# Kernel tuning notes

Measured on AMD Instinct MI355X. Metric: run time of the kernel, lower is better.

Reference implementation:

```python
import jax, jax.numpy as jnp
import numpy as np

LRELU_ALPHA = 0.2
ACT_GAIN = float(np.sqrt(2.0))  # def_gain for lrelu in bias_act
UP = 2


def setup_inputs() -> dict:
    key = jax.random.key(0)
    ks = jax.random.split(key, 5)
    B, IC, OC, WD, RES, K = 16, 512, 512, 512, 64, 3
    Hin = RES // UP
    x = jax.random.normal(ks[0], (B, IC, Hin, Hin), jnp.float32)
    w = jax.random.normal(ks[1], (B, WD), jnp.float32)
    affine_weight = jax.random.normal(ks[2], (IC, WD), jnp.float32)  # torch.randn / lr_mult(=1)
    affine_bias = jnp.ones((IC,), jnp.float32)                        # bias_init=1
    conv_weight = jax.random.normal(ks[3], (OC, IC, K, K), jnp.float32)
    bias = jnp.zeros((OC,), jnp.float32)
    noise_const = jax.random.normal(ks[4], (RES, RES), jnp.float32)
    # setup_filter([1,3,3,1]): outer product, normalized to sum 1
    f1 = jnp.array([1.0, 3.0, 3.0, 1.0], jnp.float32)
    f = jnp.outer(f1, f1)
    f = f / jnp.sum(f)
    return dict(x=x, w=w, affine_weight=affine_weight, affine_bias=affine_bias,
                conv_weight=conv_weight, bias=bias, noise_const=noise_const, f=f)


def reference(x, w, affine_weight, affine_bias, conv_weight, bias, noise_const, f):
    B, IC, H, W = x.shape
    OC, _, kh, kw = conv_weight.shape
    # --- affine (FullyConnectedLayer, linear activation) ---
    wg = 1.0 / jnp.sqrt(jnp.asarray(affine_weight.shape[1], jnp.float32))
    styles = w @ (affine_weight * wg).T + affine_bias  # [B, IC]
    # --- modulate + demodulate ---
    wmod = conv_weight[None] * styles[:, None, :, None, None]      # [B,OC,IC,kh,kw]
    dcoefs = jax.lax.rsqrt(jnp.sum(jnp.square(wmod), axis=(2, 3, 4)) + 1e-8)  # [B,OC]
    wmod = wmod * dcoefs[:, :, None, None, None]
    # --- grouped (per-sample) transpose conv, stride=UP ---
    # torch conv_transpose2d(x, W[in,out], stride=up, pad=0) ==
    # dilated cross-correlation with spatially flipped OIHW kernel, pad k-1.
    wflip = jnp.flip(wmod, (3, 4))  # [B,OC,IC,kh,kw]

    def one_sample(xb, wb):
        return jax.lax.conv_general_dilated(
            xb[None], wb, window_strides=(1, 1),
            padding=[(kh - 1, kh - 1), (kw - 1, kw - 1)],
            lhs_dilation=(UP, UP),
            dimension_numbers=('NCHW', 'OIHW', 'NCHW'))[0]

    y = jax.vmap(one_sample)(x, wflip)  # [B, OC, UP*H+1, UP*W+1]
    # --- upfirdn2d: pad 1 each side, 4x4 FIR (symmetric -> flip is identity), gain=UP^2 ---
    fh, fw = f.shape
    pad = 1  # px0 = k//2 + (fw+UP-1)//2 - (kw-1) = 1 (same for all sides)
    yp = jnp.pad(y, ((0, 0), (0, 0), (pad, pad), (pad, pad)))
    Hy, Wy = yp.shape[2], yp.shape[3]
    fk = (f * (UP * UP))[None, None]  # [1,1,fh,fw]
    y = jax.lax.conv_general_dilated(
        yp.reshape(B * OC, 1, Hy, Wy), fk, (1, 1), 'VALID',
        dimension_numbers=('NCHW', 'OIHW', 'NCHW'))
    y = y.reshape(B, OC, Hy - fh + 1, Wy - fw + 1)  # [B, OC, UP*H, UP*W]
    # --- noise (const) + bias + lrelu * gain (conv_clamp=None) ---
    y = y + noise_const[None, None]
    y = y + bias[None, :, None, None]
    y = jax.nn.leaky_relu(y, LRELU_ALPHA) * ACT_GAIN
    return y
```

## Files before the change

kernel.cpp:

```cpp
#include <hip/hip_runtime.h>
#include <hip/hip_bf16.h>
#include <cstddef>
#include <cstdint>


typedef __attribute__((ext_vector_type(8))) short s16x8;
typedef __attribute__((ext_vector_type(4))) short s16x4;
typedef __attribute__((ext_vector_type(4))) float f32x4;

static __device__ __forceinline__ unsigned short f2bf(float v) {
  __hip_bfloat16 h = __float2bfloat16(v);
  return __builtin_bit_cast(unsigned short, h);
}
static __device__ __forceinline__ float bf2f(unsigned short u) {
  unsigned int x = ((unsigned int)u) << 16;
  return __builtin_bit_cast(float, x);
}

static __device__ __forceinline__ void gload16(const void* g, const void* l) {
  __builtin_amdgcn_global_load_lds((const __attribute__((address_space(1))) unsigned int*)g,
                                   (__attribute__((address_space(3))) unsigned int*)l, 16, 0, 0);
}

__global__ void k_styles(const float* __restrict__ w, const float* __restrict__ aw,
                         const float* __restrict__ ab, float* __restrict__ styles) {
  int b = blockIdx.x;
  int ic = blockIdx.y * 32 + (threadIdx.x >> 3);
  int l = threadIdx.x & 7;
  const float wg = 0.044194173824159216f;
  const float* wp = w + b * 512 + l * 64;
  const float* ap = aw + (size_t)ic * 512 + l * 64;
  float s = 0.f;
  for (int d = 0; d < 64; d += 4) {
    float4 wv = *(const float4*)(wp + d);
    float4 av = *(const float4*)(ap + d);
    s += wv.x * av.x + wv.y * av.y + wv.z * av.z + wv.w * av.w;
  }
  s += __shfl_down(s, 4, 64);
  s += __shfl_down(s, 2, 64);
  s += __shfl_down(s, 1, 64);
  if (l == 0) styles[b * 512 + ic] = s * wg + ab[ic];
}

__global__ void k_wt_dcoef(const float* __restrict__ cw, const float* __restrict__ styles,
                           unsigned short* __restrict__ wt, float* __restrict__ dcoefs,
                           int do_wt) {
  __shared__ float lw[4608];
  __shared__ float part[4][16];
  int oc = blockIdx.x, t = threadIdx.x;
  for (int k = t; k < 4608; k += 256) lw[k] = cw[(size_t)oc * 4608 + k];
  __syncthreads();
  if (do_wt) {
    for (int c = t; c < 576; c += 256) {
      int tap = c >> 6, icc = c & 63;
      s16x8 v;
#pragma unroll
      for (int e = 0; e < 8; ++e) v[e] = (short)f2bf(lw[(icc * 8 + e) * 9 + tap]);
      *(s16x8*)(wt + ((size_t)oc * 9 + tap) * 512 + icc * 8) = v;
    }
  }
  float acc[16];
#pragma unroll
  for (int b2 = 0; b2 < 16; ++b2) acc[b2] = 0.f;
#pragma unroll
  for (int j = 0; j < 2; ++j) {
    int ic = t * 2 + j;
    float s2 = 0.f;
#pragma unroll
    for (int k = 0; k < 9; ++k) { float v = lw[ic * 9 + k]; s2 += v * v; }
#pragma unroll
    for (int b2 = 0; b2 < 16; ++b2) { float s = styles[b2 * 512 + ic]; acc[b2] += s2 * s * s; }
  }
#pragma unroll
  for (int off = 32; off > 0; off >>= 1) {
#pragma unroll
    for (int b2 = 0; b2 < 16; ++b2) acc[b2] += __shfl_down(acc[b2], off, 64);
  }
  int wid = t >> 6, lane = t & 63;
  if (lane == 0) {
    for (int b2 = 0; b2 < 16; ++b2) part[wid][b2] = acc[b2];
  }
  __syncthreads();
  if (t < 16) {
    float s = part[0][t] + part[1][t] + part[2][t] + part[3][t];
    dcoefs[t * 512 + oc] = rsqrtf(s + 1e-8f);
  }
}

__global__ void k_xt(const float* __restrict__ x, const float* __restrict__ styles,
                     unsigned short* __restrict__ xtp) {
  __shared__ __align__(16) unsigned short trans[32][520];
  int pr = blockIdx.x, b = blockIdx.y, t = threadIdx.x;
  bool interior = (pr >= 2 && pr < 34);
  if (interior) {
    int iy = pr - 2;
#pragma unroll 4
    for (int i = 0; i < 64; ++i) {
      int idx = t + i * 256;
      int ic = idx >> 5, ix = idx & 31;
      float v = x[((size_t)(b * 512 + ic)) * 1024 + iy * 32 + ix] * styles[b * 512 + ic];
      trans[ix][ic] = f2bf(v);
    }
  }
  __syncthreads();
  for (int c = t; c < 2304; c += 256) {
    int pc = c >> 6, icc = c & 63;
    s16x8 v = {0, 0, 0, 0, 0, 0, 0, 0};
    if (interior && pc >= 2 && pc < 34) v = *(const s16x8*)&trans[pc - 2][icc * 8];
    *(s16x8*)(xtp + ((size_t)(b * 1296 + pr * 36 + pc)) * 512 + icc * 8) = v;
  }
}

template <int PRE>
__global__ __launch_bounds__(256, 2)
void k_main(const unsigned short* __restrict__ xtp, const unsigned short* __restrict__ wtp,
            const float* __restrict__ xg, const float* __restrict__ cw,
            const float* __restrict__ styles, const float* __restrict__ dcoefs,
            const float* __restrict__ bias, const float* __restrict__ noise,
            float* __restrict__ out) {
  __shared__ __align__(16) unsigned char smem[58368];

  int bid = blockIdx.x;
  int q8 = (bid >> 3) + (bid & 7) * 128;
  const int ocT = q8 & 15, yT = (q8 >> 4) & 3, b = q8 >> 6;
  const int oc0 = ocT * 32;
  const int J0 = yT * 8, Y0 = yT * 16;
  const int tid = threadIdx.x, wid = tid >> 6, lane = tid & 63;
  const int l15 = lane & 15, l4 = lane >> 4;

  const int fs1 = (wid < 2) ? wid * 6 : 12 + (wid - 2) * 5;
  const int NF1 = (wid < 2) ? 6 : 5;
  int bb0[5], bb1[6];
#pragma unroll
  for (int f = 0; f < 5; ++f) {
    int n = (wid * 5 + f) * 16 + l15;
    int jy = n / 34, jx = n - jy * 34;
    bb0[f] = ((jy + 1) * 36 + jx + 1) * 80 + l4 * 16;
  }
#pragma unroll
  for (int f = 0; f < 6; ++f) {
    int n = (fs1 + f) * 16 + l15;
    int jy = n / 34, jx = n - jy * 34;
    bb1[f] = ((jy + 1) * 36 + jx + 1) * 80 + l4 * 16;
  }
  const int aoffB = l15 * 80 + l4 * 16;

  f32x4 acc0[2][2][5];
  f32x4 acc1[2][2][6];
#pragma unroll
  for (int px = 0; px < 2; ++px)
#pragma unroll
    for (int mf = 0; mf < 2; ++mf) {
#pragma unroll
      for (int f = 0; f < 5; ++f) acc0[px][mf][f] = (f32x4){0.f, 0.f, 0.f, 0.f};
#pragma unroll
      for (int f = 0; f < 6; ++f) acc1[px][mf][f] = (f32x4){0.f, 0.f, 0.f, 0.f};
    }

  const char* LX = (const char*)smem;
  const char* LW = (const char*)smem + 34816;

  for (int kc = 0; kc < 16; ++kc) {
    const int ic0 = kc * 32;
    __syncthreads();
    if (PRE) {
      const unsigned short* xsb = xtp + ((size_t)(b * 1296 + J0 * 36)) * 512 + ic0;
      for (int i = wid; i < 34; i += 4) {
        int q = i * 64 + lane;
        int q2 = q < 2159 ? q : 2159;
        int run = q2 / 5;
        int c = q2 - run * 5; c = c > 3 ? 3 : c;
        gload16(xsb + run * 512 + c * 8, smem + i * 1024);
      }
      const unsigned short* wsb = wtp + (size_t)oc0 * 4608 + ic0;
      for (int i = wid; i < 23; i += 4) {
        int q = i * 64 + lane;
        int q2 = q < 1439 ? q : 1439;
        int run = q2 / 5;
        int c = q2 - run * 5; c = c > 3 ? 3 : c;
        int tap = run >> 5, ocr = run & 31;
        gload16(wsb + (size_t)ocr * 4608 + tap * 512 + c * 8, smem + 34816 + i * 1024);
      }
      asm volatile("s_waitcnt vmcnt(0)" ::: "memory");
    } else {
      for (int s = tid; s < 1728; s += 256) {
        int run = s >> 2, c = s & 3;
        int r = run / 36, cc = run - r * 36;
        int iy = J0 + r - 2, ix = cc - 2;
        s16x8 v = {0, 0, 0, 0, 0, 0, 0, 0};
        if ((unsigned)iy < 32u && (unsigned)ix < 32u) {
#pragma unroll
          for (int e = 0; e < 8; ++e) {
            int ic = ic0 + c * 8 + e;
            v[e] = (short)f2bf(xg[((size_t)(b * 512 + ic)) * 1024 + iy * 32 + ix] * styles[b * 512 + ic]);
          }
        }
        *(s16x8*)((char*)smem + run * 80 + c * 16) = v;
      }
      for (int s = tid; s < 1152; s += 256) {
        int run = s >> 2, c = s & 3;
        int tap = run >> 5, ocr = run & 31;
        s16x8 v;
#pragma unroll
        for (int e = 0; e < 8; ++e)
          v[e] = (short)f2bf(cw[((size_t)(oc0 + ocr) * 512 + ic0 + c * 8 + e) * 9 + tap]);
        *(s16x8*)((char*)smem + 34816 + run * 80 + c * 16) = v;
      }
    }
    __syncthreads();

    const char* aw_ = LW + aoffB;
    {
      s16x8 A[3][2];
#pragma unroll
      for (int kx = 0; kx < 3; ++kx)
#pragma unroll
        for (int mf = 0; mf < 2; ++mf) A[kx][mf] = *(const s16x8*)(aw_ + kx * 2560 + mf * 1280);
#pragma unroll
      for (int f = 0; f < 5; ++f) {
        const char* bp = LX + bb0[f];
        s16x8 B3 = *(const s16x8*)(bp + 2880);
        s16x8 B4 = *(const s16x8*)(bp + 2960);
#pragma unroll
        for (int mf = 0; mf < 2; ++mf) {
          acc0[0][mf][f] = __builtin_amdgcn_mfma_f32_16x16x32_bf16(A[0][mf], B4, acc0[0][mf][f], 0, 0, 0);
          acc0[0][mf][f] = __builtin_amdgcn_mfma_f32_16x16x32_bf16(A[2][mf], B3, acc0[0][mf][f], 0, 0, 0);
          acc0[1][mf][f] = __builtin_amdgcn_mfma_f32_16x16x32_bf16(A[1][mf], B3, acc0[1][mf][f], 0, 0, 0);
        }
      }
    }
    {
      s16x8 A[3][2];
#pragma unroll
      for (int kx = 0; kx < 3; ++kx)
#pragma unroll
        for (int mf = 0; mf < 2; ++mf) A[kx][mf] = *(const s16x8*)(aw_ + (6 + kx) * 2560 + mf * 1280);
#pragma unroll
      for (int f = 0; f < 5; ++f) {
        const char* bp = LX + bb0[f];
        s16x8 B1 = *(const s16x8*)(bp);
        s16x8 B2 = *(const s16x8*)(bp + 80);
#pragma unroll
        for (int mf = 0; mf < 2; ++mf) {
          acc0[0][mf][f] = __builtin_amdgcn_mfma_f32_16x16x32_bf16(A[0][mf], B2, acc0[0][mf][f], 0, 0, 0);
          acc0[0][mf][f] = __builtin_amdgcn_mfma_f32_16x16x32_bf16(A[2][mf], B1, acc0[0][mf][f], 0, 0, 0);
          acc0[1][mf][f] = __builtin_amdgcn_mfma_f32_16x16x32_bf16(A[1][mf], B1, acc0[1][mf][f], 0, 0, 0);
        }
      }
    }
    {
      s16x8 A[3][2];
#pragma unroll
      for (int kx = 0; kx < 3; ++kx)
#pragma unroll
        for (int mf = 0; mf < 2; ++mf) A[kx][mf] = *(const s16x8*)(aw_ + (3 + kx) * 2560 + mf * 1280);
#pragma unroll
      for (int f = 0; f < 6; ++f) {
        if (f < NF1) {
          const char* bp = LX + bb1[f];
          s16x8 B1 = *(const s16x8*)(bp);
          s16x8 B2 = *(const s16x8*)(bp + 80);
#pragma unroll
          for (int mf = 0; mf < 2; ++mf) {
            acc1[0][mf][f] = __builtin_amdgcn_mfma_f32_16x16x32_bf16(A[0][mf], B2, acc1[0][mf][f], 0, 0, 0);
            acc1[0][mf][f] = __builtin_amdgcn_mfma_f32_16x16x32_bf16(A[2][mf], B1, acc1[0][mf][f], 0, 0, 0);
            acc1[1][mf][f] = __builtin_amdgcn_mfma_f32_16x16x32_bf16(A[1][mf], B1, acc1[1][mf][f], 0, 0, 0);
          }
        }
      }
    }
  }

  unsigned short* ly = (unsigned short*)smem;
#pragma unroll
  for (int mf = 0; mf < 2; ++mf) {
    __syncthreads();
#pragma unroll
    for (int f = 0; f < 5; ++f) {
      int n = (wid * 5 + f) * 16 + l15;
      if (n < 306) {
        int jy = n / 34, jx = n - jy * 34;
        int yr = 2 * jy + 1;
#pragma unroll
        for (int px = 0; px < 2; ++px) {
          int yc = 2 * jx + 1 - px;
#pragma unroll
          for (int r = 0; r < 4; ++r)
            ly[(l4 * 4 + r) * 1292 + yr * 68 + yc] = f2bf(acc0[px][mf][f][r]);
        }
      }
    }
#pragma unroll
    for (int f = 0; f < 6; ++f) {
      if (f < NF1) {
        int n = (fs1 + f) * 16 + l15;
        if (n < 340) {
          int jy = n / 34, jx = n - jy * 34;
          int yr = 2 * jy;
#pragma unroll
          for (int px = 0; px < 2; ++px) {
            int yc = 2 * jx + 1 - px;
#pragma unroll
            for (int r = 0; r < 4; ++r)
              ly[(l4 * 4 + r) * 1292 + yr * 68 + yc] = f2bf(acc1[px][mf][f][r]);
          }
        }
      }
    }
    __syncthreads();
    for (int task = tid; task < 1088; task += 256) {
      int ocr = task / 68;
      int c2 = task - ocr * 68;
      unsigned short* colp = ly + ocr * 1292 + c2;
      float y0 = bf2f(colp[0]), y1 = bf2f(colp[68]), y2 = bf2f(colp[136]);
      float vt[16];
#pragma unroll
      for (int Y = 0; Y < 16; ++Y) {
        float y3 = bf2f(colp[(Y + 3) * 68]);
        vt[Y] = 0.25f * (y0 + y3) + 0.75f * (y1 + y2);
        y0 = y1; y1 = y2; y2 = y3;
      }
#pragma unroll
      for (int Y = 0; Y < 16; ++Y) colp[Y * 68] = f2bf(vt[Y]);
    }
    __syncthreads();
    for (int task = tid; task < 1024; task += 256) {
      int ocr = task >> 6, rem = task & 63;
      int Y = rem >> 2, qq = rem & 3;
      const unsigned short* rowp = ly + ocr * 1292 + Y * 68 + qq * 16;
      float vb[20];
#pragma unroll
      for (int k = 0; k < 5; ++k) {
        s16x4 ch = *(const s16x4*)(rowp + k * 4);
#pragma unroll
        for (int j2 = 0; j2 < 4; ++j2) vb[k * 4 + j2] = bf2f((unsigned short)ch[j2]);
      }
      int oc = oc0 + mf * 16 + ocr;
      int Yg = Y0 + Y, Xg = qq * 16;
      float dc = dcoefs[b * 512 + oc];
      float bv = bias[oc];
      const float* np = noise + Yg * 64 + Xg;
      float* op = out + (((size_t)(b * 512 + oc)) * 64 + Yg) * 64 + Xg;
#pragma unroll
      for (int xx = 0; xx < 16; ++xx) {
        float o = 0.25f * (vb[xx] + vb[xx + 3]) + 0.75f * (vb[xx + 1] + vb[xx + 2]);
        o = o * dc + np[xx] + bv;
        o = (o > 0.f ? o : 0.2f * o) * 1.4142135623730951f;
        op[xx] = o;
      }
    }
  }
}

extern "C" void kernel_launch(void* const* d_in, const int* in_sizes, int n_in,
                              void* d_out, int out_size, void* d_ws, size_t ws_size,
                              hipStream_t stream) {
  const float* x = (const float*)d_in[0];
  const float* w = (const float*)d_in[1];
  const float* aw = (const float*)d_in[2];
  const float* ab = (const float*)d_in[3];
  const float* cw = (const float*)d_in[4];
  const float* bias = (const float*)d_in[5];
  const float* noise = (const float*)d_in[6];
  float* out = (float*)d_out;

  float* styles = (float*)d_ws;
  float* dcoefs = styles + 8192;
  unsigned short* xtp = (unsigned short*)((char*)d_ws + 65536);
  unsigned short* wtp = xtp + (size_t)16 * 1296 * 512;
  size_t need = 65536 + (size_t)16 * 1296 * 512 * 2 + (size_t)512 * 9 * 512 * 2;
  int pre = (ws_size >= need) ? 1 : 0;

  k_styles<<<dim3(16, 16), 256, 0, stream>>>(w, aw, ab, styles);
  k_wt_dcoef<<<dim3(512), 256, 0, stream>>>(cw, styles, wtp, dcoefs, pre);
  if (pre) {
    k_xt<<<dim3(36, 16), 256, 0, stream>>>(x, styles, xtp);
    k_main<1><<<dim3(1024), 256, 0, stream>>>(xtp, wtp, x, cw, styles, dcoefs, bias, noise, out);
  } else {
    k_main<0><<<dim3(1024), 256, 0, stream>>>(xtp, wtp, x, cw, styles, dcoefs, bias, noise, out);
  }
}
```

Measured before the change: 305.4 us.

## Double-buffer activation tiles and load weights directly from fragment-ordered global layout

The main conv kernel now double-buffers the X tile in LDS, issuing the next channel chunk's async global-to-LDS loads while MFMAs run on the current chunk. Weights are no longer staged through LDS; the prep kernel writes them in an MFMA-fragment-ordered layout so each lane loads its A operand straight from global memory. Smaller changes vectorise the x transpose loads and the vertical FIR pass, which now processes two columns per 32-bit access. LDS use grows to about 69 KB, which may limit occupancy to two blocks per CU. The direct global weight loads add latency inside the compute loop.

```diff
diff --git a/kernel.cpp b/kernel.cpp
--- a/kernel.cpp
+++ b/kernel.cpp
@@ -42,21 +42,23 @@
   if (l == 0) styles[b * 512 + ic] = s * wg + ab[ic];
 }
 
-__global__ void k_wt_dcoef(const float* __restrict__ cw, const float* __restrict__ styles,
-                           unsigned short* __restrict__ wt, float* __restrict__ dcoefs,
-                           int do_wt) {
+__global__ void k_prep(const float* __restrict__ cw, const float* __restrict__ styles,
+                       unsigned short* __restrict__ wt2, float* __restrict__ dcoefs,
+                       int do_wt) {
   __shared__ float lw[4608];
   __shared__ float part[4][16];
   int oc = blockIdx.x, t = threadIdx.x;
-  for (int k = t; k < 4608; k += 256) lw[k] = cw[(size_t)oc * 4608 + k];
+  for (int k = t; k < 1152; k += 256)
+    *(float4*)(lw + k * 4) = *(const float4*)(cw + (size_t)oc * 4608 + k * 4);
   __syncthreads();
   if (do_wt) {
+    int ocT = oc >> 5, mf = (oc >> 4) & 1, l15 = oc & 15;
     for (int c = t; c < 576; c += 256) {
-      int tap = c >> 6, icc = c & 63;
+      int kc = c / 36, rem = c % 36, tap = rem >> 2, l4 = rem & 3;
       s16x8 v;
 #pragma unroll
-      for (int e = 0; e < 8; ++e) v[e] = (short)f2bf(lw[(icc * 8 + e) * 9 + tap]);
-      *(s16x8*)(wt + ((size_t)oc * 9 + tap) * 512 + icc * 8) = v;
+      for (int e = 0; e < 8; ++e) v[e] = (short)f2bf(lw[(kc * 32 + l4 * 8 + e) * 9 + tap]);
+      *(s16x8*)(wt2 + ((size_t)(((ocT * 16 + kc) * 9 + tap) * 2 + mf) * 64 + l4 * 16 + l15) * 8) = v;
     }
   }
   float acc[16];
@@ -94,12 +96,14 @@
   bool interior = (pr >= 2 && pr < 34);
   if (interior) {
     int iy = pr - 2;
-#pragma unroll 4
-    for (int i = 0; i < 64; ++i) {
-      int idx = t + i * 256;
-      int ic = idx >> 5, ix = idx & 31;
-      float v = x[((size_t)(b * 512 + ic)) * 1024 + iy * 32 + ix] * styles[b * 512 + ic];
-      trans[ix][ic] = f2bf(v);
+    for (int task = t; task < 4096; task += 256) {
+      int ic = task >> 3, q = task & 7;
+      float4 v = *(const float4*)(x + ((size_t)(b * 512 + ic)) * 1024 + iy * 32 + q * 4);
+      float s = styles[b * 512 + ic];
+      trans[q * 4 + 0][ic] = f2bf(v.x * s);
+      trans[q * 4 + 1][ic] = f2bf(v.y * s);
+      trans[q * 4 + 2][ic] = f2bf(v.z * s);
+      trans[q * 4 + 3][ic] = f2bf(v.w * s);
     }
   }
   __syncthreads();
@@ -113,12 +117,12 @@
 
 template <int PRE>
 __global__ __launch_bounds__(256, 2)
-void k_main(const unsigned short* __restrict__ xtp, const unsigned short* __restrict__ wtp,
+void k_main(const unsigned short* __restrict__ xtp, const unsigned short* __restrict__ wt2,
             const float* __restrict__ xg, const float* __restrict__ cw,
             const float* __restrict__ styles, const float* __restrict__ dcoefs,
             const float* __restrict__ bias, const float* __restrict__ noise,
             float* __restrict__ out) {
-  __shared__ __align__(16) unsigned char smem[58368];
+  __shared__ __align__(16) unsigned char smem[69120];
 
   int bid = blockIdx.x;
   int q8 = (bid >> 3) + (bid & 7) * 128;
@@ -143,7 +147,6 @@
     int jy = n / 34, jx = n - jy * 34;
     bb1[f] = ((jy + 1) * 36 + jx + 1) * 80 + l4 * 16;
   }
-  const int aoffB = l15 * 80 + l4 * 16;
 
   f32x4 acc0[2][2][5];
   f32x4 acc1[2][2][6];
@@ -157,32 +160,35 @@
       for (int f = 0; f < 6; ++f) acc1[px][mf][f] = (f32x4){0.f, 0.f, 0.f, 0.f};
     }
 
-  const char* LX = (const char*)smem;
-  const char* LW = (const char*)smem + 34816;
+  const unsigned short* xsb = xtp + ((size_t)(b * 1296 + J0 * 36)) * 512;
+
+  if (PRE) {
+    for (int i = wid; i < 34; i += 4) {
+      int q = i * 64 + lane;
+      int q2 = q < 2159 ? q : 2159;
+      int run = q2 / 5;
+      int c = q2 - run * 5; c = c > 3 ? 3 : c;
+      gload16(xsb + run * 512 + c * 8, smem + i * 1024);
+    }
+    __syncthreads();
+  }
 
   for (int kc = 0; kc < 16; ++kc) {
     const int ic0 = kc * 32;
-    __syncthreads();
     if (PRE) {
-      const unsigned short* xsb = xtp + ((size_t)(b * 1296 + J0 * 36)) * 512 + ic0;
-      for (int i = wid; i < 34; i += 4) {
-        int q = i * 64 + lane;
-        int q2 = q < 2159 ? q : 2159;
-        int run = q2 / 5;
-        int c = q2 - run * 5; c = c > 3 ? 3 : c;
-        gload16(xsb + run * 512 + c * 8, smem + i * 1024);
-      }
-      const unsigned short* wsb = wtp + (size_t)oc0 * 4608 + ic0;
-      for (int i = wid; i < 23; i += 4) {
-        int q = i * 64 + lane;
-        int q2 = q < 1439 ? q : 1439;
-        int run = q2 / 5;
-        int c = q2 - run * 5; c = c > 3 ? 3 : c;
-        int tap = run >> 5, ocr = run & 31;
-        gload16(wsb + (size_t)ocr * 4608 + tap * 512 + c * 8, smem + 34816 + i * 1024);
-      }
-      asm volatile("s_waitcnt vmcnt(0)" ::: "memory");
+      if (kc < 15) {
+        char* dst = (char*)smem + ((kc + 1) & 1) * 34560;
+        const unsigned short* src = xsb + (kc + 1) * 32;
+        for (int i = wid; i < 34; i += 4) {
+          int q = i * 64 + lane;
+          int q2 = q < 2159 ? q : 2159;
+          int run = q2 / 5;
+          int c = q2 - run * 5; c = c > 3 ? 3 : c;
+          gload16(src + run * 512 + c * 8, dst + i * 1024);
+        }
+      }
     } else {
+      __syncthreads();
       for (int s = tid; s < 1728; s += 256) {
         int run = s >> 2, c = s & 3;
         int r = run / 36, cc = run - r * 36;
@@ -197,28 +203,34 @@
         }
         *(s16x8*)((char*)smem + run * 80 + c * 16) = v;
       }
-      for (int s = tid; s < 1152; s += 256) {
-        int run = s >> 2, c = s & 3;
-        int tap = run >> 5, ocr = run & 31;
-        s16x8 v;
-#pragma unroll
-        for (int e = 0; e < 8; ++e)
-          v[e] = (short)f2bf(cw[((size_t)(oc0 + ocr) * 512 + ic0 + c * 8 + e) * 9 + tap]);
-        *(s16x8*)((char*)smem + 34816 + run * 80 + c * 16) = v;
-      }
-    }
-    __syncthreads();
-
-    const char* aw_ = LW + aoffB;
+      __syncthreads();
+    }
+
+    const char* BUF = (const char*)smem + (PRE ? (kc & 1) * 34560 : 0);
+    const unsigned short* aB = wt2 + ((size_t)(ocT * 16 + kc)) * 9 * 1024 + lane * 8;
+
+#define LOAD_A(A, TAP0)                                                                   \
+    {                                                                                     \
+      if (PRE) {                                                                          \
+        _Pragma("unroll") for (int kx = 0; kx < 3; ++kx)                                  \
+          _Pragma("unroll") for (int mf = 0; mf < 2; ++mf)                                \
+            A[kx][mf] = *(const s16x8*)(aB + ((TAP0 + kx) * 2 + mf) * 512);               \
+      } else {                                                                            \
+        _Pragma("unroll") for (int kx = 0; kx < 3; ++kx)                                  \
+          _Pragma("unroll") for (int mf = 0; mf < 2; ++mf) {                              \
+            _Pragma("unroll") for (int e = 0; e < 8; ++e)                                 \
+              A[kx][mf][e] = (short)f2bf(                                                 \
+                  cw[((size_t)(oc0 + mf * 16 + l15) * 512 + ic0 + l4 * 8 + e) * 9 + TAP0 + kx]); \
+          }                                                                               \
+      }                                                                                   \
+    }
+
     {
       s16x8 A[3][2];
-#pragma unroll
-      for (int kx = 0; kx < 3; ++kx)
-#pragma unroll
-        for (int mf = 0; mf < 2; ++mf) A[kx][mf] = *(const s16x8*)(aw_ + kx * 2560 + mf * 1280);
+      LOAD_A(A, 0)
 #pragma unroll
       for (int f = 0; f < 5; ++f) {
-        const char* bp = LX + bb0[f];
+        const char* bp = BUF + bb0[f];
         s16x8 B3 = *(const s16x8*)(bp + 2880);
         s16x8 B4 = *(const s16x8*)(bp + 2960);
 #pragma unroll
@@ -231,13 +243,10 @@
     }
     {
       s16x8 A[3][2];
-#pragma unroll
-      for (int kx = 0; kx < 3; ++kx)
-#pragma unroll
-        for (int mf = 0; mf < 2; ++mf) A[kx][mf] = *(const s16x8*)(aw_ + (6 + kx) * 2560 + mf * 1280);
+      LOAD_A(A, 6)
 #pragma unroll
       for (int f = 0; f < 5; ++f) {
-        const char* bp = LX + bb0[f];
+        const char* bp = BUF + bb0[f];
         s16x8 B1 = *(const s16x8*)(bp);
         s16x8 B2 = *(const s16x8*)(bp + 80);
 #pragma unroll
@@ -250,14 +259,11 @@
     }
     {
       s16x8 A[3][2];
-#pragma unroll
-      for (int kx = 0; kx < 3; ++kx)
-#pragma unroll
-        for (int mf = 0; mf < 2; ++mf) A[kx][mf] = *(const s16x8*)(aw_ + (3 + kx) * 2560 + mf * 1280);
+      LOAD_A(A, 3)
 #pragma unroll
       for (int f = 0; f < 6; ++f) {
         if (f < NF1) {
-          const char* bp = LX + bb1[f];
+          const char* bp = BUF + bb1[f];
           s16x8 B1 = *(const s16x8*)(bp);
           s16x8 B2 = *(const s16x8*)(bp + 80);
 #pragma unroll
@@ -269,6 +275,8 @@
         }
       }
     }
+#undef LOAD_A
+    if (PRE) __syncthreads();
   }
 
   unsigned short* ly = (unsigned short*)smem;
@@ -308,20 +316,22 @@
       }
     }
     __syncthreads();
-    for (int task = tid; task < 1088; task += 256) {
-      int ocr = task / 68;
-      int c2 = task - ocr * 68;
-      unsigned short* colp = ly + ocr * 1292 + c2;
-      float y0 = bf2f(colp[0]), y1 = bf2f(colp[68]), y2 = bf2f(colp[136]);
-      float vt[16];
+    for (int task = tid; task < 544; task += 256) {
+      int ocr = task / 34, cp = task - ocr * 34;
+      unsigned int* colp = (unsigned int*)(ly + ocr * 1292) + cp;
+      unsigned int u0 = colp[0], u1 = colp[34], u2 = colp[68];
 #pragma unroll
       for (int Y = 0; Y < 16; ++Y) {
-        float y3 = bf2f(colp[(Y + 3) * 68]);
-        vt[Y] = 0.25f * (y0 + y3) + 0.75f * (y1 + y2);
-        y0 = y1; y1 = y2; y2 = y3;
-      }
-#pragma unroll
-      for (int Y = 0; Y < 16; ++Y) colp[Y * 68] = f2bf(vt[Y]);
+        unsigned int u3 = colp[(Y + 3) * 34];
+        float a0 = bf2f((unsigned short)(u0 & 0xffff)), b0 = bf2f((unsigned short)(u0 >> 16));
+        float a1 = bf2f((unsigned short)(u1 & 0xffff)), b1 = bf2f((unsigned short)(u1 >> 16));
+        float a2 = bf2f((unsigned short)(u2 & 0xffff)), b2 = bf2f((unsigned short)(u2 >> 16));
+        float a3 = bf2f((unsigned short)(u3 & 0xffff)), b3 = bf2f((unsigned short)(u3 >> 16));
+        float va = 0.25f * (a0 + a3) + 0.75f * (a1 + a2);
+        float vb = 0.25f * (b0 + b3) + 0.75f * (b1 + b2);
+        colp[Y * 34] = (unsigned int)f2bf(va) | ((unsigned int)f2bf(vb) << 16);
+        u0 = u1; u1 = u2; u2 = u3;
+      }
     }
     __syncthreads();
     for (int task = tid; task < 1024; task += 256) {
@@ -367,16 +377,16 @@
   float* styles = (float*)d_ws;
   float* dcoefs = styles + 8192;
   unsigned short* xtp = (unsigned short*)((char*)d_ws + 65536);
-  unsigned short* wtp = xtp + (size_t)16 * 1296 * 512;
-  size_t need = 65536 + (size_t)16 * 1296 * 512 * 2 + (size_t)512 * 9 * 512 * 2;
+  unsigned short* wt2 = xtp + (size_t)16 * 1296 * 512;
+  size_t need = 65536 + (size_t)16 * 1296 * 512 * 2 + (size_t)16 * 16 * 9 * 1024 * 2;
   int pre = (ws_size >= need) ? 1 : 0;
 
   k_styles<<<dim3(16, 16), 256, 0, stream>>>(w, aw, ab, styles);
-  k_wt_dcoef<<<dim3(512), 256, 0, stream>>>(cw, styles, wtp, dcoefs, pre);
+  k_prep<<<dim3(512), 256, 0, stream>>>(cw, styles, wt2, dcoefs, pre);
   if (pre) {
     k_xt<<<dim3(36, 16), 256, 0, stream>>>(x, styles, xtp);
-    k_main<1><<<dim3(1024), 256, 0, stream>>>(xtp, wtp, x, cw, styles, dcoefs, bias, noise, out);
+    k_main<1><<<dim3(1024), 256, 0, stream>>>(xtp, wt2, x, cw, styles, dcoefs, bias, noise, out);
   } else {
-    k_main<0><<<dim3(1024), 256, 0, stream>>>(xtp, wtp, x, cw, styles, dcoefs, bias, noise, out);
-  }
-}
+    k_main<0><<<dim3(1024), 256, 0, stream>>>(xtp, wt2, x, cw, styles, dcoefs, bias, noise, out);
+  }
+}
```

New measurement: 313.9 us. +2.8%, slower.
